# Kernel optimization log

Measured on AMD Instinct MI355X. Metric: run time of the kernel, lower is better.

Reference implementation:

```python
import jax, jax.numpy as jnp
import numpy as np

B, T, E, H = 2, 2048, 1024, 16
HD = E // H
EPS = 1e-5


def layer_norm(x, g, b):
    mu = jnp.mean(x, axis=-1, keepdims=True)
    var = jnp.mean(jnp.square(x - mu), axis=-1, keepdims=True)
    return (x - mu) * jax.lax.rsqrt(var + EPS) * g + b


def setup_inputs() -> dict:
    key = jax.random.key(0)
    ks = jax.random.split(key, 12)
    s = 0.02
    return {
        "x": jax.random.normal(ks[0], (B, T, E), jnp.float32),
        "Wk": jax.random.normal(ks[1], (E, E), jnp.float32) * s,
        "Wq": jax.random.normal(ks[2], (E, E), jnp.float32) * s,
        "Wv": jax.random.normal(ks[3], (E, E), jnp.float32) * s,
        "Wp": jax.random.normal(ks[4], (E, E), jnp.float32) * s,
        "bp": jnp.zeros((E,), jnp.float32),
        "W1": jax.random.normal(ks[5], (E, 4 * E), jnp.float32) * s,
        "b1": jnp.zeros((4 * E,), jnp.float32),
        "W2": jax.random.normal(ks[6], (4 * E, E), jnp.float32) * s,
        "b2": jnp.zeros((E,), jnp.float32),
        "g1": jnp.ones((E,), jnp.float32),
        "be1": jnp.zeros((E,), jnp.float32),
        "g2": jnp.ones((E,), jnp.float32),
        "be2": jnp.zeros((E,), jnp.float32),
    }


def reference(x, Wk, Wq, Wv, Wp, bp, W1, b1, W2, b2, g1, be1, g2, be2):
    # --- attention sublayer ---
    h = layer_norm(x, g1, be1)
    q = (h @ Wq).reshape(B, T, H, HD).transpose(0, 2, 1, 3)  # [B,H,T,HD]
    k = (h @ Wk).reshape(B, T, H, HD).transpose(0, 2, 1, 3)
    v = (h @ Wv).reshape(B, T, H, HD).transpose(0, 2, 1, 3)
    scores = jnp.einsum('bhqd,bhkd->bhqk', q, k) * (HD ** -0.5)
    causal = jnp.tril(jnp.ones((T, T), bool))
    scores = jnp.where(causal, scores, -jnp.inf)
    probs = jax.nn.softmax(scores, axis=-1)  # dropout is identity (eval)
    attn = jnp.einsum('bhqk,bhkd->bhqd', probs, v)
    attn = attn.transpose(0, 2, 1, 3).reshape(B, T, E)
    x = x + attn @ Wp + bp
    # --- FFN sublayer ---
    h2 = layer_norm(x, g2, be2)
    ff = jax.nn.relu(h2 @ W1 + b1) @ W2 + b2
    return x + ff
```

## Files before the change

kernel.cpp:

```cpp
#include <hip/hip_runtime.h>
#include <hip/hip_bf16.h>

#define B_ 2
#define T_ 2048
#define E_ 1024
#define H_ 16
#define HD_ 64
#define NT (B_*T_)

typedef __attribute__((ext_vector_type(8))) short s16x8;
typedef __attribute__((ext_vector_type(4))) float f32x4;

using bf16 = __hip_bfloat16;

#define MFMA16(a,b,c) __builtin_amdgcn_mfma_f32_16x16x32_bf16(a,b,c,0,0,0)

__device__ inline unsigned short f2bf(float f) {
    bf16 h = __float2bfloat16(f);
    return *reinterpret_cast<unsigned short*>(&h);
}

__device__ __forceinline__ float bf2f(unsigned short u) {
    unsigned x = ((unsigned)u) << 16;
    return __uint_as_float(x);
}

__device__ __forceinline__ unsigned cvt_pk_bf16(float lo, float hi) {
    unsigned r;
    asm("v_cvt_pk_bf16_f32 %0, %1, %2" : "=v"(r) : "v"(lo), "v"(hi));
    return r;
}

__device__ __forceinline__ float exp2_fast(float x) {
    float r;
    asm("v_exp_f32 %0, %1" : "=v"(r) : "v"(x));
    return r;
}

__device__ __forceinline__ void async_cp16(const void* g, void* l) {
    __builtin_amdgcn_global_load_lds((const __attribute__((address_space(1))) void*)g,
                                     (__attribute__((address_space(3))) void*)l,
                                     16, 0, 0);
}

__global__ __launch_bounds__(256) void transpose_all(const float* __restrict__ Wq,
                                                     const float* __restrict__ Wk,
                                                     const float* __restrict__ Wv,
                                                     const float* __restrict__ Wp,
                                                     const float* __restrict__ W1,
                                                     const float* __restrict__ W2,
                                                     bf16* __restrict__ Wqkv_t,
                                                     bf16* __restrict__ W1_t,
                                                     bf16* __restrict__ W2_t) {
    __shared__ float tile[32][33];
    int id = blockIdx.x;
    const float* src; bf16* dst; int K, N, n0, k0;
    float scl = 1.0f;
    if (id < 4096) {
        int z = id >> 10, t = id & 1023;
        src = z == 0 ? Wq : z == 1 ? Wk : z == 2 ? Wv : Wp;
        if (z == 0) scl = 0.125f * 1.44269504088896f;
        dst = Wqkv_t + (size_t)z * 1048576;
        K = 1024; N = 1024; n0 = (t & 31) * 32; k0 = (t >> 5) * 32;
    } else if (id < 8192) {
        int t = id - 4096; src = W1; dst = W1_t; K = 1024; N = 4096;
        n0 = (t & 127) * 32; k0 = (t >> 7) * 32;
    } else {
        int t = id - 8192; src = W2; dst = W2_t; K = 4096; N = 1024;
        n0 = (t & 31) * 32; k0 = (t >> 5) * 32;
    }
    int tx = threadIdx.x, ty = threadIdx.y;
#pragma unroll
    for (int i = 0; i < 4; ++i)
        tile[ty + i*8][tx] = src[(size_t)(k0 + ty + i*8)*N + n0 + tx];
    __syncthreads();
#pragma unroll
    for (int i = 0; i < 4; ++i)
        dst[(size_t)(n0 + ty + i*8)*K + k0 + tx] = __float2bfloat16(tile[tx][ty + i*8] * scl);
}

__global__ __launch_bounds__(256) void ln_kernel(const float* __restrict__ x,
                                                 const float* __restrict__ g,
                                                 const float* __restrict__ b,
                                                 bf16* __restrict__ h) {
    int row = blockIdx.x;
    int tid = threadIdx.x;
    const float4 xv = *reinterpret_cast<const float4*>(x + (size_t)row*E_ + tid*4);
    float s  = xv.x + xv.y + xv.z + xv.w;
    float sq = xv.x*xv.x + xv.y*xv.y + xv.z*xv.z + xv.w*xv.w;
#pragma unroll
    for (int o = 32; o > 0; o >>= 1) { s += __shfl_xor(s, o); sq += __shfl_xor(sq, o); }
    __shared__ float red[8];
    int w = tid >> 6, lane = tid & 63;
    if (lane == 0) { red[w] = s; red[4 + w] = sq; }
    __syncthreads();
    float S = red[0] + red[1] + red[2] + red[3];
    float Q = red[4] + red[5] + red[6] + red[7];
    float mu = S * (1.0f/E_);
    float var = Q * (1.0f/E_) - mu*mu;
    float rs = rsqrtf(var + 1e-5f);
    const float4 gv = *reinterpret_cast<const float4*>(g + tid*4);
    const float4 bv = *reinterpret_cast<const float4*>(b + tid*4);
    ushort4 o4;
    o4.x = f2bf((xv.x - mu)*rs*gv.x + bv.x);
    o4.y = f2bf((xv.y - mu)*rs*gv.y + bv.y);
    o4.z = f2bf((xv.z - mu)*rs*gv.z + bv.z);
    o4.w = f2bf((xv.w - mu)*rs*gv.w + bv.w);
    *reinterpret_cast<ushort4*>(h + (size_t)row*E_ + tid*4) = o4;
}

__global__ __launch_bounds__(256) void ln_kernel_b(const bf16* __restrict__ x,
                                                   const float* __restrict__ g,
                                                   const float* __restrict__ b,
                                                   bf16* __restrict__ h) {
    int row = blockIdx.x;
    int tid = threadIdx.x;
    ushort4 u4 = *reinterpret_cast<const ushort4*>(x + (size_t)row*E_ + tid*4);
    float v0 = bf2f(u4.x), v1 = bf2f(u4.y), v2 = bf2f(u4.z), v3 = bf2f(u4.w);
    float s  = v0 + v1 + v2 + v3;
    float sq = v0*v0 + v1*v1 + v2*v2 + v3*v3;
#pragma unroll
    for (int o = 32; o > 0; o >>= 1) { s += __shfl_xor(s, o); sq += __shfl_xor(sq, o); }
    __shared__ float red[8];
    int w = tid >> 6, lane = tid & 63;
    if (lane == 0) { red[w] = s; red[4 + w] = sq; }
    __syncthreads();
    float S = red[0] + red[1] + red[2] + red[3];
    float Q = red[4] + red[5] + red[6] + red[7];
    float mu = S * (1.0f/E_);
    float var = Q * (1.0f/E_) - mu*mu;
    float rs = rsqrtf(var + 1e-5f);
    const float4 gv = *reinterpret_cast<const float4*>(g + tid*4);
    const float4 bv = *reinterpret_cast<const float4*>(b + tid*4);
    ushort4 o4;
    o4.x = f2bf((v0 - mu)*rs*gv.x + bv.x);
    o4.y = f2bf((v1 - mu)*rs*gv.y + bv.y);
    o4.z = f2bf((v2 - mu)*rs*gv.z + bv.z);
    o4.w = f2bf((v3 - mu)*rs*gv.w + bv.w);
    *reinterpret_cast<ushort4*>(h + (size_t)row*E_ + tid*4) = o4;
}

template<int BM, int BN, int EPI>
__global__ __launch_bounds__(256)
void gemm_t(const bf16* __restrict__ A, const bf16* __restrict__ Bt, void* Cout,
            const float* __restrict__ bias, const void* res,
            int M, int N, int K) {
    constexpr int MT = BM / 32;
    constexpr int NB = BN / 32;
    constexpr int MHALF = BM / 2, NHALF = BN / 2;
    __shared__ bf16 As[BM*64];
    __shared__ bf16 Bs[BN*64];
    int tid = threadIdx.x;
    int lane = tid & 63, w = tid >> 6;
    int wr = w >> 1, wc = w & 1;
    int nbx = gridDim.x;
    int hid = blockIdx.y * nbx + blockIdx.x;
    int cpx = (nbx * gridDim.y) >> 3;
    int nid = (hid & 7) * cpx + (hid >> 3);
    int m0 = (nid / nbx) * BM, n0 = (nid % nbx) * BN;
    int lr = lane & 15, lq = lane >> 4;
    f32x4 acc[MT][NB] = {};
    int srow = w*8 + (lane >> 3);
    int schunk = ((lane & 7) ^ (srow & 7)) * 8;
    const bf16* Ap = A  + (size_t)(m0 + srow)*K + schunk;
    const bf16* Bp = Bt + (size_t)(n0 + srow)*K + schunk;
    for (int k0 = 0; k0 < K; k0 += 64) {
#pragma unroll
        for (int i = 0; i < BM/32; ++i)
            async_cp16(Ap + (size_t)(i*32)*K + k0, (char*)As + i*4096 + w*1024);
#pragma unroll
        for (int i = 0; i < BN/32; ++i)
            async_cp16(Bp + (size_t)(i*32)*K + k0, (char*)Bs + i*4096 + w*1024);
        __syncthreads();
        const char* Asb = (const char*)As;
        const char* Bsb = (const char*)Bs;
        s16x8 af[2][MT], bfr[2][NB];
#pragma unroll
        for (int m = 0; m < MT; ++m) {
            int row = wr*MHALF + m*16 + lr;
            int base = row*128, sw = (row & 7) << 4;
#pragma unroll
            for (int kk = 0; kk < 2; ++kk)
                af[kk][m] = *reinterpret_cast<const s16x8*>(Asb + base + ((kk*64 + lq*16) ^ sw));
        }
#pragma unroll
        for (int n = 0; n < NB; ++n) {
            int row = wc*NHALF + n*16 + lr;
            int base = row*128, sw = (row & 7) << 4;
#pragma unroll
            for (int kk = 0; kk < 2; ++kk)
                bfr[kk][n] = *reinterpret_cast<const s16x8*>(Bsb + base + ((kk*64 + lq*16) ^ sw));
        }
        __builtin_amdgcn_s_setprio(1);
#pragma unroll
        for (int kk = 0; kk < 2; ++kk)
#pragma unroll
            for (int m = 0; m < MT; ++m)
#pragma unroll
                for (int n = 0; n < NB; ++n)
                    acc[m][n] = MFMA16(af[kk][m], bfr[kk][n], acc[m][n]);
        __builtin_amdgcn_s_setprio(0);
        __syncthreads();
    }
#pragma unroll
    for (int m = 0; m < MT; ++m) {
#pragma unroll
        for (int n = 0; n < NB; ++n) {
            int col = n0 + wc*NHALF + n*16 + lr;
#pragma unroll
            for (int r = 0; r < 4; ++r) {
                int row = m0 + wr*MHALF + m*16 + lq*4 + r;
                size_t idx = (size_t)row*N + col;
                float v = acc[m][n][r] + bias[col];
                if (EPI == 1) {
                    reinterpret_cast<float*>(Cout)[idx] =
                        v + reinterpret_cast<const float*>(res)[idx];
                } else if (EPI == 3) {
                    reinterpret_cast<bf16*>(Cout)[idx] =
                        __float2bfloat16(v + reinterpret_cast<const float*>(res)[idx]);
                } else {
                    reinterpret_cast<float*>(Cout)[idx] =
                        v + bf2f(reinterpret_cast<const unsigned short*>(res)[idx]);
                }
            }
        }
    }
}

#define RD(p) (*reinterpret_cast<const s16x8*>(p))
#define MM(m,n) do { acc[m][n] = MFMA16(af[m][0], bfr[n][0], acc[m][n]); \
                     acc[m][n] = MFMA16(af[m][1], bfr[n][1], acc[m][n]); } while (0)
#define MFMAS_0 MM(0,0); MM(1,0);
#define MFMAS_1 MM(2,0); MM(3,0); MM(2,1); MM(3,1); MM(0,1); MM(1,1);
#define MFMAS_2 MM(4,0); MM(5,0); MM(4,1); MM(5,1); MM(4,2); MM(5,2); \
                MM(0,2); MM(1,2); MM(2,2); MM(3,2);
#define MFMAS_3 MM(6,0); MM(7,0); MM(6,1); MM(7,1); MM(6,2); MM(7,2); \
                MM(6,3); MM(7,3); MM(0,3); MM(1,3); MM(2,3); MM(3,3); \
                MM(4,3); MM(5,3);

template<int EPI>
__global__ __launch_bounds__(512)
void gemm8p(const bf16* __restrict__ A, const bf16* __restrict__ Bt, void* Cout,
            const float* __restrict__ bias, int M, int N, int K) {
    __shared__ char smem[131072];
    int tid = threadIdx.x;
    int lane = tid & 63, w = tid >> 6;
    int wm = w >> 2, wn = w & 3;
    int nbx = gridDim.x;
    int hid = blockIdx.y * nbx + blockIdx.x;
    int cpx = (nbx * gridDim.y) >> 3;
    int nid = (hid & 7) * cpx + (hid >> 3);
    int m0 = (nid / nbx) * 256, n0 = (nid % nbx) * 256;
    int lr = lane & 15, lq = lane >> 4;
    f32x4 acc[8][4] = {};
    int srow = tid >> 3;
    int schunk = ((tid & 7) ^ (srow & 7)) * 8;
    const bf16* ApS = A  + (size_t)(m0 + srow)*K + schunk;
    const bf16* BpS = Bt + (size_t)(n0 + srow)*K + schunk;
    int sw4 = (lr & 7) << 4;
    int x0 = (lq*16) ^ sw4, x1 = (64 + lq*16) ^ sw4;
    int aoff[8], boff[4];
#pragma unroll
    for (int m = 0; m < 8; ++m)
        aoff[m] = ((m >> 1)*64 + wm*32 + (m & 1)*16 + lr) * 128;
#pragma unroll
    for (int n = 0; n < 4; ++n)
        boff[n] = (n*64 + wn*16 + lr) * 128;
    int nst = K >> 6;
    s16x8 af[8][2], bfr[4][2];
#pragma unroll
    for (int q = 0; q < 4; ++q) {
        async_cp16(ApS + (size_t)(q*64)*K, smem + q*8192 + w*1024);
        async_cp16(BpS + (size_t)(q*64)*K, smem + 32768 + q*8192 + w*1024);
    }
    ApS += 64; BpS += 64;
    asm volatile("s_waitcnt vmcnt(6)" ::: "memory");
    __builtin_amdgcn_sched_barrier(0);
    __builtin_amdgcn_s_barrier();
    __builtin_amdgcn_sched_barrier(0);

#define PHASE(Q) do {                                                              \
    af[2*Q][0]   = RD(bufA + aoff[2*Q]   + x0);                                    \
    af[2*Q][1]   = RD(bufA + aoff[2*Q]   + x1);                                    \
    af[2*Q+1][0] = RD(bufA + aoff[2*Q+1] + x0);                                    \
    af[2*Q+1][1] = RD(bufA + aoff[2*Q+1] + x1);                                    \
    bfr[Q][0]    = RD(bufB + boff[Q] + x0);                                        \
    bfr[Q][1]    = RD(bufB + boff[Q] + x1);                                        \
    if (more) {                                                                    \
        async_cp16(ApS + (size_t)(Q*64)*K, stA + Q*8192 + w*1024);                 \
        async_cp16(BpS + (size_t)(Q*64)*K, stA + 32768 + Q*8192 + w*1024);         \
        asm volatile("s_waitcnt vmcnt(6)" ::: "memory");                           \
    } else {                                                                       \
        if (Q == 0) asm volatile("s_waitcnt vmcnt(4)" ::: "memory");               \
        else if (Q == 1) asm volatile("s_waitcnt vmcnt(2)" ::: "memory");          \
        else if (Q == 2) asm volatile("s_waitcnt vmcnt(0)" ::: "memory");          \
    }                                                                              \
    __builtin_amdgcn_sched_barrier(0);                                             \
    __builtin_amdgcn_s_barrier();                                                  \
    __builtin_amdgcn_sched_barrier(0);                                             \
    asm volatile("s_waitcnt lgkmcnt(0)" ::: "memory");                             \
    __builtin_amdgcn_sched_barrier(0);                                             \
    __builtin_amdgcn_s_setprio(1);                                                 \
    MFMAS_##Q                                                                      \
    __builtin_amdgcn_s_setprio(0);                                                 \
    __builtin_amdgcn_sched_barrier(0);                                             \
    __builtin_amdgcn_s_barrier();                                                  \
    __builtin_amdgcn_sched_barrier(0);                                             \
} while (0)

    for (int t = 0; t < nst; ++t) {
        const char* bufA = smem + (size_t)(t & 1)*65536;
        const char* bufB = bufA + 32768;
        char* stA = smem + (size_t)((t & 1) ^ 1)*65536;
        bool more = (t + 1 < nst);
        PHASE(0);
        PHASE(1);
        PHASE(2);
        PHASE(3);
        ApS += 64; BpS += 64;
    }
#undef PHASE
#pragma unroll
    for (int m = 0; m < 8; ++m) {
#pragma unroll
        for (int n = 0; n < 4; ++n) {
            int col = n0 + n*64 + wn*16 + lr;
#pragma unroll
            for (int r = 0; r < 4; ++r) {
                int row = m0 + (m >> 1)*64 + wm*32 + (m & 1)*16 + lq*4 + r;
                float v = acc[m][n][r];
                if (EPI == 0) {
                    reinterpret_cast<bf16*>(Cout)[(size_t)row*N + col] = __float2bfloat16(v);
                } else {
                    v += bias[col];
                    v = v > 0.f ? v : 0.f;
                    reinterpret_cast<bf16*>(Cout)[(size_t)row*N + col] = __float2bfloat16(v);
                }
            }
        }
    }
}

__global__ __launch_bounds__(256) void v_transpose(const bf16* __restrict__ qkv,
                                                   bf16* __restrict__ Vt) {
    __shared__ unsigned short tile[32][33];
    int tx = threadIdx.x, ty = threadIdx.y;
    int bh = blockIdx.z;
    int b = bh >> 4, h = bh & 15;
    int t0 = blockIdx.x * 32, d0 = blockIdx.y * 32;
    const unsigned short* src = reinterpret_cast<const unsigned short*>(qkv);
#pragma unroll
    for (int i = 0; i < 4; ++i)
        tile[ty + i*8][tx] = src[(size_t)(b*T_ + t0 + ty + i*8)*3072 + 2048 + h*64 + d0 + tx];
    __syncthreads();
    unsigned short* dst = reinterpret_cast<unsigned short*>(Vt);
#pragma unroll
    for (int i = 0; i < 4; ++i)
        dst[(size_t)(bh*64 + d0 + ty + i*8)*T_ + t0 + tx] = tile[tx][ty + i*8];
}

__global__ __launch_bounds__(256)
void flash_attn(const bf16* __restrict__ qkv, const bf16* __restrict__ Vt,
                bf16* __restrict__ O) {
    __shared__ char smem[40960];
    int tid = threadIdx.x;
    int lane = tid & 63, w = tid >> 6;
    int lr = lane & 15, lq = lane >> 4;
    int bh = blockIdx.y, b = bh >> 4, h = bh & 15;
    int pm = (bh & 15) ^ ((bh & 16) ? 31 : 0);
    int qt = (int)(blockIdx.x ^ pm) & 31;
    int q0 = qt * 64;
    int qw = q0 + w * 16;
    const bf16* Qb = qkv + (size_t)(b*T_)*3072 + h*HD_;
    const bf16* Kb = Qb + 1024;
    const bf16* Vb = Vt + (size_t)bh * HD_ * T_;
    char* Pw = smem + 32768 + w*2048;

    int srow_ = w*8 + (lane >> 3);
    int sc_   = (((lane & 7) ^ (srow_ & 7))) * 8;
    const bf16* kS0 = Kb + (size_t)srow_*3072 + sc_;
    const bf16* kS1 = kS0 + (size_t)32*3072;
    const bf16* vS0 = Vb + (size_t)srow_*2048 + sc_;
    const bf16* vS1 = vS0 + (size_t)32*2048;
    char* kD = smem + w*1024;
    char* vD = smem + 16384 + w*1024;

    int sw4 = (lr & 7) << 4;
    int kvo[4], pwo[4];
#pragma unroll
    for (int n = 0; n < 4; ++n) {
        kvo[n] = n*2048 + lr*128 + ((lq << 4) ^ sw4);
        pwo[n] = (lr*128 + n*32 + lq*8) ^ sw4;
    }
    int pao0 = (lr*128 + lq*16) ^ sw4;
    int pao1 = (lr*128 + 64 + lq*16) ^ sw4;

    s16x8 qf[2];
#pragma unroll
    for (int kk = 0; kk < 2; ++kk)
        qf[kk] = *reinterpret_cast<const s16x8*>(Qb + (size_t)(qw + lr)*3072 + kk*32 + lq*8);
    f32x4 od[4] = {};
    const f32x4 Z4 = {0.f, 0.f, 0.f, 0.f};
    float lrun = 0.f;
    int ntiles = qt + 1;

    auto stageNext = [&](int bufi) {
        async_cp16(kS0, kD + bufi*8192);
        async_cp16(kS1, kD + bufi*8192 + 4096);
        async_cp16(vS0, vD + bufi*8192);
        async_cp16(vS1, vD + bufi*8192 + 4096);
        kS0 += 64*3072; kS1 += 64*3072; vS0 += 64; vS1 += 64;
    };

    auto step = [&](const char* Kt, const char* Vtl, bool diag, int kv0) {
        f32x4 sc[4];
        __builtin_amdgcn_s_setprio(1);
#pragma unroll
        for (int n = 0; n < 4; ++n) {
            s16x8 kf0 = *reinterpret_cast<const s16x8*>(Kt + kvo[n]);
            s16x8 kf1 = *reinterpret_cast<const s16x8*>(Kt + (kvo[n] ^ 64));
            f32x4 z = MFMA16(kf0, qf[0], Z4);
            z = MFMA16(kf1, qf[1], z);
            sc[n] = z;
        }
        __builtin_amdgcn_s_setprio(0);
        if (diag) {
            int q = qw + lr;
#pragma unroll
            for (int n = 0; n < 4; ++n)
#pragma unroll
                for (int r = 0; r < 4; ++r)
                    if (kv0 + n*16 + lq*4 + r > q) sc[n][r] = -1e30f;
        }
        float psum = 0.f;
#pragma unroll
        for (int n = 0; n < 4; ++n) {
            float p0 = exp2_fast(sc[n][0]);
            float p1 = exp2_fast(sc[n][1]);
            float p2 = exp2_fast(sc[n][2]);
            float p3 = exp2_fast(sc[n][3]);
            psum += (p0 + p1) + (p2 + p3);
            uint2 pk;
            pk.x = cvt_pk_bf16(p0, p1);
            pk.y = cvt_pk_bf16(p2, p3);
            *reinterpret_cast<uint2*>(Pw + pwo[n]) = pk;
        }
        psum += __shfl_xor(psum, 16);
        psum += __shfl_xor(psum, 32);
        lrun += psum;
        asm volatile("" ::: "memory");
        s16x8 pa0 = *reinterpret_cast<const s16x8*>(Pw + pao0);
        s16x8 pa1 = *reinterpret_cast<const s16x8*>(Pw + pao1);
        __builtin_amdgcn_s_setprio(1);
#pragma unroll
        for (int nd = 0; nd < 4; ++nd) {
            s16x8 vf0 = *reinterpret_cast<const s16x8*>(Vtl + kvo[nd]);
            s16x8 vf1 = *reinterpret_cast<const s16x8*>(Vtl + (kvo[nd] ^ 64));
            od[nd] = MFMA16(pa0, vf0, od[nd]);
            od[nd] = MFMA16(pa1, vf1, od[nd]);
        }
        __builtin_amdgcn_s_setprio(0);
    };

    stageNext(0);
    for (int it = 0; it < ntiles - 1; ++it) {
        int curb = it & 1;
        stageNext(curb ^ 1);
        asm volatile("s_waitcnt vmcnt(4)" ::: "memory");
        __builtin_amdgcn_sched_barrier(0);
        __builtin_amdgcn_s_barrier();
        __builtin_amdgcn_sched_barrier(0);
        step(smem + curb*8192, smem + 16384 + curb*8192, false, 0);
        __builtin_amdgcn_sched_barrier(0);
        __builtin_amdgcn_s_barrier();
        __builtin_amdgcn_sched_barrier(0);
    }
    {
        int curb = (ntiles - 1) & 1;
        asm volatile("s_waitcnt vmcnt(0)" ::: "memory");
        __builtin_amdgcn_sched_barrier(0);
        __builtin_amdgcn_s_barrier();
        __builtin_amdgcn_sched_barrier(0);
        step(smem + curb*8192, smem + 16384 + curb*8192, true, (ntiles - 1) * 64);
    }
    float lR[4];
#pragma unroll
    for (int r = 0; r < 4; ++r) lR[r] = 1.0f / __shfl(lrun, lq*4 + r);
#pragma unroll
    for (int nd = 0; nd < 4; ++nd) {
#pragma unroll
        for (int r = 0; r < 4; ++r) {
            int row = qw + lq*4 + r;
            O[(size_t)(b*T_ + row)*E_ + h*HD_ + nd*16 + lr] = __float2bfloat16(od[nd][r] * lR[r]);
        }
    }
}

extern "C" void kernel_launch(void* const* d_in, const int* in_sizes, int n_in,
                              void* d_out, int out_size, void* d_ws, size_t ws_size,
                              hipStream_t stream) {
    const float* x   = (const float*)d_in[0];
    const float* Wk  = (const float*)d_in[1];
    const float* Wq  = (const float*)d_in[2];
    const float* Wv  = (const float*)d_in[3];
    const float* Wp  = (const float*)d_in[4];
    const float* bp  = (const float*)d_in[5];
    const float* W1  = (const float*)d_in[6];
    const float* b1  = (const float*)d_in[7];
    const float* W2  = (const float*)d_in[8];
    const float* b2  = (const float*)d_in[9];
    const float* g1  = (const float*)d_in[10];
    const float* be1 = (const float*)d_in[11];
    const float* g2  = (const float*)d_in[12];
    const float* be2 = (const float*)d_in[13];
    float* out = (float*)d_out;

    char* ws = (char*)d_ws;
    bf16* Wqkv_t = (bf16*)(ws + 0);
    bf16* Wp_t   = (bf16*)(ws + 6291456);
    bf16* W1_t   = (bf16*)(ws + 8388608);
    bf16* W2_t   = (bf16*)(ws + 16777216);
    bf16* h      = (bf16*)(ws + 25165824);
    bf16* qkv    = (bf16*)(ws + 33554432);
    bf16* Vt     = (bf16*)(ws + 58720256);
    bf16* attnO  = (bf16*)(ws + 67108864);
    bf16* ff1    = (bf16*)(ws + 33554432);
    bool big = ws_size >= 83886080;
    bf16* x2b = (bf16*)(ws + 75497472);

    dim3 tb(32, 8);
    transpose_all<<<12288, tb, 0, stream>>>(Wq, Wk, Wv, Wp, W1, W2, Wqkv_t, W1_t, W2_t);

    ln_kernel<<<NT, 256, 0, stream>>>(x, g1, be1, h);
    gemm8p<0><<<dim3(12, 16), 512, 0, stream>>>(h, Wqkv_t, qkv, nullptr, NT, 3072, 1024);
    v_transpose<<<dim3(64, 2, 32), tb, 0, stream>>>(qkv, Vt);
    flash_attn<<<dim3(32, 32), 256, 0, stream>>>(qkv, Vt, attnO);
    if (big) {
        gemm_t<64,64,3><<<dim3(16, 64), 256, 0, stream>>>(attnO, Wp_t, x2b, bp, x, NT, 1024, 1024);
        ln_kernel_b<<<NT, 256, 0, stream>>>(x2b, g2, be2, h);
        gemm8p<2><<<dim3(16, 16), 512, 0, stream>>>(h, W1_t, ff1, b1, NT, 4096, 1024);
        gemm_t<64,64,4><<<dim3(16, 64), 256, 0, stream>>>(ff1, W2_t, out, b2, x2b, NT, 1024, 4096);
    } else {
        gemm_t<64,64,1><<<dim3(16, 64), 256, 0, stream>>>(attnO, Wp_t, out, bp, x, NT, 1024, 1024);
        ln_kernel<<<NT, 256, 0, stream>>>(out, g2, be2, h);
        gemm8p<2><<<dim3(16, 16), 512, 0, stream>>>(h, W1_t, ff1, b1, NT, 4096, 1024);
        gemm_t<64,64,1><<<dim3(16, 64), 256, 0, stream>>>(ff1, W2_t, out, b2, out, NT, 1024, 4096);
    }
}
```

Measured before the change: 198.0 us.

## Restructure 256x256 GEMM into quadrant-based ping-pong schedule with staggered prefetch

Replaces the four-phase 8-wave GEMM with a variant where each wave owns a contiguous 128x64 output region and computes it in four quadrant passes. A operands are prefetched one K-step ahead and B operands two steps ahead, with the loads spread across the passes. This halves the A fragment registers and interleaves global loads with MFMA blocks to hide memory latency better. It changes the warp-to-output mapping and the waitcnt accounting, which risks bank conflicts or pipeline hazards if the counts are wrong.

New measurement: 199.9 us. No clear change (+0.9%).

```diff
diff --git a/kernel.cpp b/kernel.cpp
--- a/kernel.cpp
+++ b/kernel.cpp
@@ -14,6 +14,7 @@
 using bf16 = __hip_bfloat16;
 
 #define MFMA16(a,b,c) __builtin_amdgcn_mfma_f32_16x16x32_bf16(a,b,c,0,0,0)
+#define RD(p) (*reinterpret_cast<const s16x8*>(p))
 
 __device__ inline unsigned short f2bf(float f) {
     bf16 h = __float2bfloat16(f);
@@ -227,20 +228,9 @@
     }
 }
 
-#define RD(p) (*reinterpret_cast<const s16x8*>(p))
-#define MM(m,n) do { acc[m][n] = MFMA16(af[m][0], bfr[n][0], acc[m][n]); \
-                     acc[m][n] = MFMA16(af[m][1], bfr[n][1], acc[m][n]); } while (0)
-#define MFMAS_0 MM(0,0); MM(1,0);
-#define MFMAS_1 MM(2,0); MM(3,0); MM(2,1); MM(3,1); MM(0,1); MM(1,1);
-#define MFMAS_2 MM(4,0); MM(5,0); MM(4,1); MM(5,1); MM(4,2); MM(5,2); \
-                MM(0,2); MM(1,2); MM(2,2); MM(3,2);
-#define MFMAS_3 MM(6,0); MM(7,0); MM(6,1); MM(7,1); MM(6,2); MM(7,2); \
-                MM(6,3); MM(7,3); MM(0,3); MM(1,3); MM(2,3); MM(3,3); \
-                MM(4,3); MM(5,3);
-
 template<int EPI>
 __global__ __launch_bounds__(512)
-void gemm8p(const bf16* __restrict__ A, const bf16* __restrict__ Bt, void* Cout,
+void gemm8q(const bf16* __restrict__ A, const bf16* __restrict__ Bt, void* Cout,
             const float* __restrict__ bias, int M, int N, int K) {
     __shared__ char smem[131072];
     int tid = threadIdx.x;
@@ -253,82 +243,142 @@
     int m0 = (nid / nbx) * 256, n0 = (nid % nbx) * 256;
     int lr = lane & 15, lq = lane >> 4;
     f32x4 acc[8][4] = {};
-    int srow = tid >> 3;
-    int schunk = ((tid & 7) ^ (srow & 7)) * 8;
-    const bf16* ApS = A  + (size_t)(m0 + srow)*K + schunk;
-    const bf16* BpS = Bt + (size_t)(n0 + srow)*K + schunk;
+    int srow = w*8 + (lane >> 3);
+    int schunk = ((lane & 7) ^ (srow & 7)) * 8;
+    const bf16* Ab = A  + (size_t)m0 * K;
+    const bf16* Bb = Bt + (size_t)n0 * K;
     int sw4 = (lr & 7) << 4;
     int x0 = (lq*16) ^ sw4, x1 = (64 + lq*16) ^ sw4;
     int aoff[8], boff[4];
 #pragma unroll
-    for (int m = 0; m < 8; ++m)
-        aoff[m] = ((m >> 1)*64 + wm*32 + (m & 1)*16 + lr) * 128;
-#pragma unroll
-    for (int n = 0; n < 4; ++n)
-        boff[n] = (n*64 + wn*16 + lr) * 128;
+    for (int mi = 0; mi < 8; ++mi) aoff[mi] = (wm*128 + mi*16 + lr)*128;
+#pragma unroll
+    for (int ni = 0; ni < 4; ++ni) boff[ni] = 32768 + (wn*64 + ni*16 + lr)*128;
     int nst = K >> 6;
-    s16x8 af[8][2], bfr[4][2];
-#pragma unroll
-    for (int q = 0; q < 4; ++q) {
-        async_cp16(ApS + (size_t)(q*64)*K, smem + q*8192 + w*1024);
-        async_cp16(BpS + (size_t)(q*64)*K, smem + 32768 + q*8192 + w*1024);
-    }
-    ApS += 64; BpS += 64;
-    asm volatile("s_waitcnt vmcnt(6)" ::: "memory");
+    s16x8 af[4][2], bfr[4][2];
+
+    auto stA2 = [&](int buf, int g0, int t) {
+        async_cp16(Ab + (size_t)(g0*64 + srow)*K + t*64 + schunk,
+                   smem + buf*65536 + g0*8192 + w*1024);
+        async_cp16(Ab + (size_t)((g0+1)*64 + srow)*K + t*64 + schunk,
+                   smem + buf*65536 + (g0+1)*8192 + w*1024);
+    };
+    auto stB2 = [&](int buf, int g0, int t) {
+        async_cp16(Bb + (size_t)(g0*64 + srow)*K + t*64 + schunk,
+                   smem + buf*65536 + 32768 + g0*8192 + w*1024);
+        async_cp16(Bb + (size_t)((g0+1)*64 + srow)*K + t*64 + schunk,
+                   smem + buf*65536 + 32768 + (g0+1)*8192 + w*1024);
+    };
+    stA2(0, 0, 0); stA2(0, 2, 0);
+    stB2(0, 0, 0); stB2(0, 2, 0);
+    stB2(1, 0, 1); stB2(1, 2, 1);
+    asm volatile("s_waitcnt vmcnt(4)" ::: "memory");
     __builtin_amdgcn_sched_barrier(0);
     __builtin_amdgcn_s_barrier();
     __builtin_amdgcn_sched_barrier(0);
 
-#define PHASE(Q) do {                                                              \
-    af[2*Q][0]   = RD(bufA + aoff[2*Q]   + x0);                                    \
-    af[2*Q][1]   = RD(bufA + aoff[2*Q]   + x1);                                    \
-    af[2*Q+1][0] = RD(bufA + aoff[2*Q+1] + x0);                                    \
-    af[2*Q+1][1] = RD(bufA + aoff[2*Q+1] + x1);                                    \
-    bfr[Q][0]    = RD(bufB + boff[Q] + x0);                                        \
-    bfr[Q][1]    = RD(bufB + boff[Q] + x1);                                        \
-    if (more) {                                                                    \
-        async_cp16(ApS + (size_t)(Q*64)*K, stA + Q*8192 + w*1024);                 \
-        async_cp16(BpS + (size_t)(Q*64)*K, stA + 32768 + Q*8192 + w*1024);         \
-        asm volatile("s_waitcnt vmcnt(6)" ::: "memory");                           \
-    } else {                                                                       \
-        if (Q == 0) asm volatile("s_waitcnt vmcnt(4)" ::: "memory");               \
-        else if (Q == 1) asm volatile("s_waitcnt vmcnt(2)" ::: "memory");          \
-        else if (Q == 2) asm volatile("s_waitcnt vmcnt(0)" ::: "memory");          \
-    }                                                                              \
-    __builtin_amdgcn_sched_barrier(0);                                             \
-    __builtin_amdgcn_s_barrier();                                                  \
-    __builtin_amdgcn_sched_barrier(0);                                             \
-    asm volatile("s_waitcnt lgkmcnt(0)" ::: "memory");                             \
-    __builtin_amdgcn_sched_barrier(0);                                             \
-    __builtin_amdgcn_s_setprio(1);                                                 \
-    MFMAS_##Q                                                                      \
-    __builtin_amdgcn_s_setprio(0);                                                 \
-    __builtin_amdgcn_sched_barrier(0);                                             \
-    __builtin_amdgcn_s_barrier();                                                  \
-    __builtin_amdgcn_sched_barrier(0);                                             \
-} while (0)
-
     for (int t = 0; t < nst; ++t) {
-        const char* bufA = smem + (size_t)(t & 1)*65536;
-        const char* bufB = bufA + 32768;
-        char* stA = smem + (size_t)((t & 1) ^ 1)*65536;
-        bool more = (t + 1 < nst);
-        PHASE(0);
-        PHASE(1);
-        PHASE(2);
-        PHASE(3);
-        ApS += 64; BpS += 64;
-    }
-#undef PHASE
-#pragma unroll
-    for (int m = 0; m < 8; ++m) {
-#pragma unroll
-        for (int n = 0; n < 4; ++n) {
-            int col = n0 + n*64 + wn*16 + lr;
+        const char* bc = smem + (size_t)(t & 1)*65536;
+        int nb = (t + 1) & 1;
+        bool s1 = (t + 1 < nst), s2 = (t + 2 < nst);
+#pragma unroll
+        for (int s = 0; s < 4; ++s) {
+            af[s][0] = RD(bc + aoff[s] + x0);
+            af[s][1] = RD(bc + aoff[s] + x1);
+        }
+#pragma unroll
+        for (int ni = 0; ni < 2; ++ni) {
+            bfr[ni][0] = RD(bc + boff[ni] + x0);
+            bfr[ni][1] = RD(bc + boff[ni] + x1);
+        }
+        if (s1) stA2(nb, 0, t + 1);
+        __builtin_amdgcn_sched_barrier(0);
+        __builtin_amdgcn_s_barrier();
+        asm volatile("s_waitcnt lgkmcnt(0)" ::: "memory");
+        __builtin_amdgcn_sched_barrier(0);
+        __builtin_amdgcn_s_setprio(1);
+#pragma unroll
+        for (int s = 0; s < 4; ++s)
+#pragma unroll
+            for (int ni = 0; ni < 2; ++ni) {
+                acc[s][ni] = MFMA16(af[s][0], bfr[ni][0], acc[s][ni]);
+                acc[s][ni] = MFMA16(af[s][1], bfr[ni][1], acc[s][ni]);
+            }
+        __builtin_amdgcn_s_setprio(0);
+        __builtin_amdgcn_sched_barrier(0);
+        __builtin_amdgcn_s_barrier();
+        __builtin_amdgcn_sched_barrier(0);
+#pragma unroll
+        for (int ni = 2; ni < 4; ++ni) {
+            bfr[ni][0] = RD(bc + boff[ni] + x0);
+            bfr[ni][1] = RD(bc + boff[ni] + x1);
+        }
+        if (s1) stA2(nb, 2, t + 1);
+        __builtin_amdgcn_sched_barrier(0);
+        __builtin_amdgcn_s_barrier();
+        asm volatile("s_waitcnt lgkmcnt(0)" ::: "memory");
+        __builtin_amdgcn_sched_barrier(0);
+        __builtin_amdgcn_s_setprio(1);
+#pragma unroll
+        for (int s = 0; s < 4; ++s)
+#pragma unroll
+            for (int ni = 2; ni < 4; ++ni) {
+                acc[s][ni] = MFMA16(af[s][0], bfr[ni][0], acc[s][ni]);
+                acc[s][ni] = MFMA16(af[s][1], bfr[ni][1], acc[s][ni]);
+            }
+        __builtin_amdgcn_s_setprio(0);
+        __builtin_amdgcn_sched_barrier(0);
+        __builtin_amdgcn_s_barrier();
+        __builtin_amdgcn_sched_barrier(0);
+#pragma unroll
+        for (int s = 0; s < 4; ++s) {
+            af[s][0] = RD(bc + aoff[4 + s] + x0);
+            af[s][1] = RD(bc + aoff[4 + s] + x1);
+        }
+        if (s2) stB2(t & 1, 0, t + 2);
+        __builtin_amdgcn_sched_barrier(0);
+        __builtin_amdgcn_s_barrier();
+        asm volatile("s_waitcnt lgkmcnt(0)" ::: "memory");
+        __builtin_amdgcn_sched_barrier(0);
+        __builtin_amdgcn_s_setprio(1);
+#pragma unroll
+        for (int s = 0; s < 4; ++s)
+#pragma unroll
+            for (int ni = 2; ni < 4; ++ni) {
+                acc[4 + s][ni] = MFMA16(af[s][0], bfr[ni][0], acc[4 + s][ni]);
+                acc[4 + s][ni] = MFMA16(af[s][1], bfr[ni][1], acc[4 + s][ni]);
+            }
+        __builtin_amdgcn_s_setprio(0);
+        __builtin_amdgcn_sched_barrier(0);
+        __builtin_amdgcn_s_barrier();
+        __builtin_amdgcn_sched_barrier(0);
+        if (s2) stB2(t & 1, 2, t + 2);
+        __builtin_amdgcn_s_setprio(1);
+#pragma unroll
+        for (int s = 0; s < 4; ++s)
+#pragma unroll
+            for (int ni = 0; ni < 2; ++ni) {
+                acc[4 + s][ni] = MFMA16(af[s][0], bfr[ni][0], acc[4 + s][ni]);
+                acc[4 + s][ni] = MFMA16(af[s][1], bfr[ni][1], acc[4 + s][ni]);
+            }
+        __builtin_amdgcn_s_setprio(0);
+        if (s1) {
+            if (s2) asm volatile("s_waitcnt vmcnt(4)" ::: "memory");
+            else    asm volatile("s_waitcnt vmcnt(0)" ::: "memory");
+        }
+        __builtin_amdgcn_sched_barrier(0);
+        __builtin_amdgcn_s_barrier();
+        __builtin_amdgcn_sched_barrier(0);
+    }
+#pragma unroll
+    for (int mi = 0; mi < 8; ++mi) {
+#pragma unroll
+        for (int ni = 0; ni < 4; ++ni) {
+            int col = n0 + wn*64 + ni*16 + lr;
 #pragma unroll
             for (int r = 0; r < 4; ++r) {
-                int row = m0 + (m >> 1)*64 + wm*32 + (m & 1)*16 + lq*4 + r;
-                float v = acc[m][n][r];
+                int row = m0 + wm*128 + mi*16 + lq*4 + r;
+                float v = acc[mi][ni][r];
                 if (EPI == 0) {
                     reinterpret_cast<bf16*>(Cout)[(size_t)row*N + col] = __float2bfloat16(v);
                 } else {
@@ -532,18 +582,18 @@
     transpose_all<<<12288, tb, 0, stream>>>(Wq, Wk, Wv, Wp, W1, W2, Wqkv_t, W1_t, W2_t);
 
     ln_kernel<<<NT, 256, 0, stream>>>(x, g1, be1, h);
-    gemm8p<0><<<dim3(12, 16), 512, 0, stream>>>(h, Wqkv_t, qkv, nullptr, NT, 3072, 1024);
+    gemm8q<0><<<dim3(12, 16), 512, 0, stream>>>(h, Wqkv_t, qkv, nullptr, NT, 3072, 1024);
     v_transpose<<<dim3(64, 2, 32), tb, 0, stream>>>(qkv, Vt);
     flash_attn<<<dim3(32, 32), 256, 0, stream>>>(qkv, Vt, attnO);
     if (big) {
         gemm_t<64,64,3><<<dim3(16, 64), 256, 0, stream>>>(attnO, Wp_t, x2b, bp, x, NT, 1024, 1024);
         ln_kernel_b<<<NT, 256, 0, stream>>>(x2b, g2, be2, h);
-        gemm8p<2><<<dim3(16, 16), 512, 0, stream>>>(h, W1_t, ff1, b1, NT, 4096, 1024);
+        gemm8q<2><<<dim3(16, 16), 512, 0, stream>>>(h, W1_t, ff1, b1, NT, 4096, 1024);
         gemm_t<64,64,4><<<dim3(16, 64), 256, 0, stream>>>(ff1, W2_t, out, b2, x2b, NT, 1024, 4096);
     } else {
         gemm_t<64,64,1><<<dim3(16, 64), 256, 0, stream>>>(attnO, Wp_t, out, bp, x, NT, 1024, 1024);
         ln_kernel<<<NT, 256, 0, stream>>>(out, g2, be2, h);
-        gemm8p<2><<<dim3(16, 16), 512, 0, stream>>>(h, W1_t, ff1, b1, NT, 4096, 1024);
+        gemm8q<2><<<dim3(16, 16), 512, 0, stream>>>(h, W1_t, ff1, b1, NT, 4096, 1024);
         gemm_t<64,64,1><<<dim3(16, 64), 256, 0, stream>>>(ff1, W2_t, out, b2, out, NT, 1024, 4096);
     }
 }
```
